# Kernel tuning notes

Measured on AMD Instinct MI355X. Metric: run time of the kernel, lower is better.

Reference implementation:

```python
import jax, jax.numpy as jnp
import numpy as np

B, N, E, H = 4, 1024, 1024, 16
D = E // H

def setup_inputs() -> dict:
    key = jax.random.key(0)
    ks = jax.random.split(key, 5)
    return {
        "x": jax.random.normal(ks[0], (B, N, E), dtype=jnp.float32),
        "Wqkv": jax.random.normal(ks[1], (E, 3 * E), dtype=jnp.float32) * 0.02,
        "bqkv": jax.random.normal(ks[2], (3 * E,), dtype=jnp.float32) * 0.02,
        "Wfc": jax.random.normal(ks[3], (E, E), dtype=jnp.float32) * 0.02,
        "bfc": jax.random.normal(ks[4], (E,), dtype=jnp.float32) * 0.02,
    }

def reference(x, Wqkv, bqkv, Wfc, bfc):
    b, n, e = x.shape
    h, d = H, E // H
    qkv = x @ Wqkv + bqkv                      # [b, n, 3e]
    q, k, v = jnp.split(qkv, 3, axis=-1)       # each [b, n, e]
    # view to [b, n, h, d] then RAW reshape to [b, h, n, d] (faithful to original,
    # which uses .reshape, not transpose — mixes seq/head axes)
    q = q.reshape(b, n, h, d).reshape(b, h, n, d)
    k = k.reshape(b, n, h, d).reshape(b, h, n, d)
    v = v.reshape(b, n, h, d).reshape(b, h, n, d)
    scores = jnp.einsum('bhqd,bhkd->bhqk', q, k) / jnp.sqrt(jnp.float32(d))
    causal = jnp.triu(jnp.ones((n, n), dtype=bool), k=1)  # True above diagonal
    scores = jnp.where(causal, -jnp.inf, scores)
    attn = jax.nn.softmax(scores, axis=-1)
    out = jnp.einsum('bhqk,bhkd->bhqd', attn, v)          # [b, h, n, d]
    # raw reshape back to [b, n, h, d] then flatten heads (faithful)
    out = out.reshape(b, n, h, d).reshape(b, n, e)
    return out @ Wfc + bfc
```

## Files before the change

kernel.cpp:

```cpp
#include <hip/hip_runtime.h>


typedef __bf16 bf16x8 __attribute__((ext_vector_type(8)));
typedef float f32x4 __attribute__((ext_vector_type(4)));

#define QSCALE 0.18033688011112042f
#define DEFER_THR 11.0f

__device__ __forceinline__ unsigned short f2bf(float f) {
    unsigned u = __float_as_uint(f);
    u += 0x7fffu + ((u >> 16) & 1u);
    return (unsigned short)(u >> 16);
}

__device__ __forceinline__ unsigned cvtpk_bf16(float lo, float hi) {
    unsigned r;
    asm("v_cvt_pk_bf16_f32 %0, %1, %2" : "=v"(r) : "v"(lo), "v"(hi));
    return r;
}

union FragU { uint4 u; bf16x8 v; };

__device__ __forceinline__ bf16x8 ld_frag(const unsigned short* p) {
    FragU x; x.u = *(const uint4*)p; return x.v;
}

__device__ __forceinline__ void gload_lds16(const void* g, void* l) {
    __builtin_amdgcn_global_load_lds(
        (const __attribute__((address_space(1))) void*)g,
        (__attribute__((address_space(3))) void*)l, 16, 0, 0);
}

__global__ __launch_bounds__(256) void prep(
    const float* __restrict__ x,    unsigned short* __restrict__ xb,
    const float* __restrict__ Wqkv, unsigned short* __restrict__ wqkvT,
    const float* __restrict__ Wfc,  unsigned short* __restrict__ wfcT)
{
    __shared__ float tile[32][33];
    int bid = blockIdx.x;
    int tx = threadIdx.x & 31, ty = threadIdx.x >> 5;
    if (bid < 3072) {
        int c0 = (bid % 96) * 32, r0 = (bid / 96) * 32;
        for (int i = ty; i < 32; i += 8)
            tile[i][tx] = Wqkv[(r0 + i) * 3072 + c0 + tx];
        __syncthreads();
        for (int i = ty; i < 32; i += 8)
            wqkvT[(long)(c0 + i) * 1024 + r0 + tx] = f2bf(tile[tx][i]);
    } else if (bid < 4096) {
        int b2 = bid - 3072;
        int c0 = (b2 % 32) * 32, r0 = (b2 / 32) * 32;
        for (int i = ty; i < 32; i += 8)
            tile[i][tx] = Wfc[(r0 + i) * 1024 + c0 + tx];
        __syncthreads();
        for (int i = ty; i < 32; i += 8)
            wfcT[(long)(c0 + i) * 1024 + r0 + tx] = f2bf(tile[tx][i]);
    } else {
        const int n4 = 1 << 20;
        for (int i = (bid - 4096) * 256 + threadIdx.x; i < n4; i += 1024 * 256) {
            float4 f = ((const float4*)x)[i];
            unsigned a = (unsigned)f2bf(f.x) | ((unsigned)f2bf(f.y) << 16);
            unsigned b = (unsigned)f2bf(f.z) | ((unsigned)f2bf(f.w) << 16);
            ((uint2*)xb)[i] = make_uint2(a, b);
        }
    }
}

__global__ void transpose_v(const unsigned short* __restrict__ v,
                            unsigned short* __restrict__ vt) {
    __shared__ unsigned short tile[32][33];
    int bh = blockIdx.z;
    int n0 = blockIdx.x * 32, d0 = blockIdx.y * 32;
    const unsigned short* src = v + (long)bh * 65536;
    unsigned short* dst = vt + (long)bh * 65536;
    for (int i = threadIdx.y; i < 32; i += 8)
        tile[i][threadIdx.x] = src[(n0 + i) * 64 + d0 + threadIdx.x];
    __syncthreads();
    for (int i = threadIdx.y; i < 32; i += 8)
        dst[(d0 + i) * 1024 + n0 + threadIdx.x] = tile[threadIdx.x][i];
}

template <int MODE>
__global__ __launch_bounds__(256) void gemm128(
    const unsigned short* __restrict__ A,
    const unsigned short* __restrict__ Bt,
    const float* __restrict__ bias,
    unsigned short* __restrict__ qb,
    unsigned short* __restrict__ kb,
    unsigned short* __restrict__ vb,
    float* __restrict__ outf)
{
    __shared__ unsigned short As[2][4096];
    __shared__ unsigned short Bs[2][4096];
    int t = threadIdx.x, lane = t & 63, w = t >> 6;
    int wm = w >> 1, wn = w & 1;
    int lrow = lane >> 4, lcol = lane & 15;

    const int NX  = (MODE == 0) ? 24 : 8;
    const int CPX = (MODE == 0) ? 96 : 32;
    int id = blockIdx.x;
    int idp = (id & 7) * CPX + (id >> 3);
    int tn0 = (idp % NX) * 128, tm0 = (idp / NX) * 128;

    int seg0 = w * 1024;
    int seg1 = (w + 4) * 1024;
    int off0 = seg0 + lane * 16, off1 = seg1 + lane * 16;
    int r0 = off0 >> 6, g0 = ((((off0 >> 4) & 3) ^ ((r0 >> 1) & 3)) << 4);
    int r1 = off1 >> 6, g1 = ((((off1 >> 4) & 3) ^ ((r1 >> 1) & 3)) << 4);

    const char* gA = (const char*)A;
    const char* gB = (const char*)Bt;

    int aoff[4], boff[4];
    #pragma unroll
    for (int mi = 0; mi < 4; ++mi) {
        int row = wm * 64 + mi * 16 + lcol;
        aoff[mi] = row * 32 + ((lrow ^ ((row >> 1) & 3)) << 3);
    }
    #pragma unroll
    for (int ni = 0; ni < 4; ++ni) {
        int row = wn * 64 + ni * 16 + lcol;
        boff[ni] = row * 32 + ((lrow ^ ((row >> 1) & 3)) << 3);
    }

    f32x4 acc[4][4] = {};

    auto STAGE = [&](int buf, int kt) {
        long kby = (long)kt * 2;
        gload_lds16(gA + (long)(tm0 + r0) * 2048 + kby + g0, (char*)&As[buf][0] + seg0);
        gload_lds16(gA + (long)(tm0 + r1) * 2048 + kby + g1, (char*)&As[buf][0] + seg1);
        gload_lds16(gB + (long)(tn0 + r0) * 2048 + kby + g0, (char*)&Bs[buf][0] + seg0);
        gload_lds16(gB + (long)(tn0 + r1) * 2048 + kby + g1, (char*)&Bs[buf][0] + seg1);
    };

    STAGE(0, 0);
    STAGE(1, 32);

    for (int tt = 0; tt < 32; ++tt) {
        if (tt < 31) asm volatile("s_waitcnt vmcnt(4)" ::: "memory");
        else         asm volatile("s_waitcnt vmcnt(0)" ::: "memory");
        __builtin_amdgcn_s_barrier();

        int cur = tt & 1;
        bf16x8 af[4], bfr[4];
        #pragma unroll
        for (int mi = 0; mi < 4; ++mi) af[mi] = ld_frag(&As[cur][aoff[mi]]);
        #pragma unroll
        for (int ni = 0; ni < 4; ++ni) bfr[ni] = ld_frag(&Bs[cur][boff[ni]]);
        #pragma unroll
        for (int mi = 0; mi < 4; ++mi)
            #pragma unroll
            for (int ni = 0; ni < 4; ++ni)
                acc[mi][ni] = __builtin_amdgcn_mfma_f32_16x16x32_bf16(af[mi], bfr[ni], acc[mi][ni], 0, 0, 0);

        __builtin_amdgcn_s_barrier();
        if (tt + 2 < 32) STAGE(cur, (tt + 2) * 32);
    }

    #pragma unroll
    for (int mi = 0; mi < 4; ++mi) {
        int gr0 = tm0 + wm * 64 + mi * 16 + lrow * 4;
        #pragma unroll
        for (int ni = 0; ni < 4; ++ni) {
            int gc = tn0 + wn * 64 + ni * 16 + lcol;
            float bv = bias[gc];
            if (MODE == 0) {
                int sec = gc >> 10, ei = gc & 1023;
                unsigned short* dst = sec == 0 ? qb : (sec == 1 ? kb : vb);
                if (sec == 0) {
                    #pragma unroll
                    for (int r = 0; r < 4; ++r)
                        dst[(long)(gr0 + r) * 1024 + ei] = f2bf((acc[mi][ni][r] + bv) * QSCALE);
                } else {
                    #pragma unroll
                    for (int r = 0; r < 4; ++r)
                        dst[(long)(gr0 + r) * 1024 + ei] = f2bf(acc[mi][ni][r] + bv);
                }
            } else {
                #pragma unroll
                for (int r = 0; r < 4; ++r)
                    outf[(long)(gr0 + r) * 1024 + gc] = acc[mi][ni][r] + bv;
            }
        }
    }
}

__global__ __launch_bounds__(256) void attn(
    const unsigned short* __restrict__ qbuf,
    const unsigned short* __restrict__ kbuf,
    const unsigned short* __restrict__ vtbuf,
    unsigned short* __restrict__ obuf)
{
    __shared__ unsigned short Ks[2][4096];
    __shared__ unsigned short Vs[2][4096];
    __shared__ unsigned short Ps[4][32][40];

    int id = blockIdx.x;
    int xcd = id & 7, s_ = id >> 3;
    int j  = 7 - (s_ >> 3);
    int bh = xcd + 8 * (s_ & 7);

    const char* Kb = (const char*)(kbuf + (long)bh * 65536);
    const char* Vb = (const char*)(vtbuf + (long)bh * 65536);
    const unsigned short* Q = qbuf + (long)bh * 65536;
    unsigned short* O = obuf + (long)bh * 65536;

    int t = threadIdx.x, lane = t & 63, w = t >> 6;
    int lrow = lane >> 4, lcol = lane & 15;
    const float NEG = -__builtin_inff();

    int qbase = j * 128 + w * 32;
    int T = 2 * j + 2;

    int row0 = w * 8 + (lane >> 3);
    int slot = (((lane & 7) ^ (lane >> 3)) << 4);

    auto STAGE = [&](int buf, int kt) {
        long k2 = (long)kt * 2;
        gload_lds16(Kb + (k2 + row0 * 2) * 64 + slot,        (char*)&Ks[buf][0] + w * 1024);
        gload_lds16(Kb + (k2 + (row0 + 32) * 2) * 64 + slot, (char*)&Ks[buf][0] + 4096 + w * 1024);
        gload_lds16(Vb + (long)row0 * 2048 + k2 + slot,        (char*)&Vs[buf][0] + w * 1024);
        gload_lds16(Vb + (long)(row0 + 32) * 2048 + k2 + slot, (char*)&Vs[buf][0] + 4096 + w * 1024);
    };

    bf16x8 qf[2][2];
    #pragma unroll
    for (int qg = 0; qg < 2; ++qg)
        #pragma unroll
        for (int kc = 0; kc < 2; ++kc)
            qf[qg][kc] = ld_frag(Q + (long)(qbase + qg * 16 + lcol) * 64 + kc * 32 + lrow * 8);

    f32x4 acc[2][4] = {};
    float m_i[2] = {NEG, NEG};
    float lsum[2][2] = {{0.f, 0.f}, {0.f, 0.f}};

    STAGE(0, 0);
    STAGE(1, 64);

    for (int tt = 0; tt < T; ++tt) {
        if (tt + 1 < T) asm volatile("s_waitcnt vmcnt(4)" ::: "memory");
        else            asm volatile("s_waitcnt vmcnt(0)" ::: "memory");
        __builtin_amdgcn_s_barrier();

        int cur = tt & 1;
        #pragma unroll
        for (int ks = 0; ks < 2; ++ks) {
            int kt_sub = tt * 64 + ks * 32;
            if (kt_sub <= qbase) {
                bf16x8 kf[2][2], vf[4];
                #pragma unroll
                for (int kg = 0; kg < 2; ++kg)
                    #pragma unroll
                    for (int kc = 0; kc < 2; ++kc) {
                        int row = ks * 32 + kg * 16 + lcol;
                        kf[kg][kc] = ld_frag(&Ks[cur][row * 64 + (((kc * 4 + lrow) ^ (row & 7)) << 3)]);
                    }
                #pragma unroll
                for (int dg = 0; dg < 4; ++dg) {
                    int row = dg * 16 + lcol;
                    vf[dg] = ld_frag(&Vs[cur][row * 64 + (((ks * 4 + lrow) ^ (row & 7)) << 3)]);
                }

                f32x4 s[2][2] = {};
                __builtin_amdgcn_s_setprio(1);
                #pragma unroll
                for (int kg = 0; kg < 2; ++kg)
                    #pragma unroll
                    for (int kc = 0; kc < 2; ++kc) {
                        s[0][kg] = __builtin_amdgcn_mfma_f32_16x16x32_bf16(kf[kg][kc], qf[0][kc], s[0][kg], 0, 0, 0);
                        s[1][kg] = __builtin_amdgcn_mfma_f32_16x16x32_bf16(kf[kg][kc], qf[1][kc], s[1][kg], 0, 0, 0);
                    }
                __builtin_amdgcn_s_setprio(0);

                bool diag = (kt_sub == qbase);
                if (diag) {
                    #pragma unroll
                    for (int qg = 0; qg < 2; ++qg)
                        #pragma unroll
                        for (int kg = 0; kg < 2; ++kg)
                            #pragma unroll
                            for (int r = 0; r < 4; ++r)
                                if (kg * 16 + lrow * 4 + r > qg * 16 + lcol)
                                    s[qg][kg][r] = NEG;
                }
                float lmax[2];
                #pragma unroll
                for (int qg = 0; qg < 2; ++qg) {
                    float a0 = fmaxf(s[qg][0][0], s[qg][0][1]), a1 = fmaxf(s[qg][0][2], s[qg][0][3]);
                    float a2 = fmaxf(s[qg][1][0], s[qg][1][1]), a3 = fmaxf(s[qg][1][2], s[qg][1][3]);
                    lmax[qg] = fmaxf(fmaxf(a0, a1), fmaxf(a2, a3));
                }
                bool ok = (lmax[0] <= m_i[0] + DEFER_THR) && (lmax[1] <= m_i[1] + DEFER_THR);
                if (!__all(ok)) {
                    #pragma unroll
                    for (int qg = 0; qg < 2; ++qg) {
                        float mx = fmaxf(lmax[qg], __shfl_xor(lmax[qg], 16));
                        mx = fmaxf(mx, __shfl_xor(mx, 32));
                        float mnew = fmaxf(m_i[qg], mx);
                        float alpha = exp2f(m_i[qg] - mnew);
                        m_i[qg] = mnew;
                        lsum[qg][0] *= alpha;
                        lsum[qg][1] *= alpha;
                        #pragma unroll
                        for (int dg = 0; dg < 4; ++dg)
                            #pragma unroll
                            for (int r = 0; r < 4; ++r)
                                acc[qg][dg][r] *= alpha;
                    }
                }
                #pragma unroll
                for (int qg = 0; qg < 2; ++qg) {
                    float p[8];
                    #pragma unroll
                    for (int kg = 0; kg < 2; ++kg)
                        #pragma unroll
                        for (int r = 0; r < 4; ++r)
                            p[kg * 4 + r] = exp2f(s[qg][kg][r] - m_i[qg]);
                    lsum[qg][0] += (p[0] + p[1]) + (p[2] + p[3]);
                    lsum[qg][1] += (p[4] + p[5]) + (p[6] + p[7]);
                    unsigned u0 = cvtpk_bf16(p[0], p[1]);
                    unsigned u1 = cvtpk_bf16(p[2], p[3]);
                    unsigned u2 = cvtpk_bf16(p[4], p[5]);
                    unsigned u3 = cvtpk_bf16(p[6], p[7]);
                    *(uint2*)&Ps[w][qg * 16 + lcol][lrow * 4]      = make_uint2(u0, u1);
                    *(uint2*)&Ps[w][qg * 16 + lcol][16 + lrow * 4] = make_uint2(u2, u3);
                }

                bf16x8 pb[2];
                pb[0] = ld_frag(&Ps[w][lcol][lrow * 8]);
                pb[1] = ld_frag(&Ps[w][16 + lcol][lrow * 8]);

                __builtin_amdgcn_s_setprio(1);
                #pragma unroll
                for (int dg = 0; dg < 4; ++dg) {
                    acc[0][dg] = __builtin_amdgcn_mfma_f32_16x16x32_bf16(vf[dg], pb[0], acc[0][dg], 0, 0, 0);
                    acc[1][dg] = __builtin_amdgcn_mfma_f32_16x16x32_bf16(vf[dg], pb[1], acc[1][dg], 0, 0, 0);
                }
                __builtin_amdgcn_s_setprio(0);
            }
        }

        __builtin_amdgcn_s_barrier();
        if (tt + 2 < T) STAGE(cur, (tt + 2) * 64);
    }

    #pragma unroll
    for (int qg = 0; qg < 2; ++qg) {
        float lr = lsum[qg][0] + lsum[qg][1];
        lr += __shfl_xor(lr, 16);
        lr += __shfl_xor(lr, 32);
        float inv = 1.f / lr;
        int q = qbase + qg * 16 + lcol;
        #pragma unroll
        for (int dg = 0; dg < 4; ++dg) {
            ushort4 pk;
            pk.x = f2bf(acc[qg][dg][0] * inv);
            pk.y = f2bf(acc[qg][dg][1] * inv);
            pk.z = f2bf(acc[qg][dg][2] * inv);
            pk.w = f2bf(acc[qg][dg][3] * inv);
            *(ushort4*)&O[(long)q * 64 + dg * 16 + lrow * 4] = pk;
        }
    }
}

extern "C" void kernel_launch(void* const* d_in, const int* in_sizes, int n_in,
                              void* d_out, int out_size, void* d_ws, size_t ws_size,
                              hipStream_t stream) {
    const float* x    = (const float*)d_in[0];
    const float* Wqkv = (const float*)d_in[1];
    const float* bqkv = (const float*)d_in[2];
    const float* Wfc  = (const float*)d_in[3];
    const float* bfc  = (const float*)d_in[4];
    float* out = (float*)d_out;

    unsigned short* ws    = (unsigned short*)d_ws;
    unsigned short* xb    = ws;
    unsigned short* wqkvT = xb + (4u << 20);
    unsigned short* wfcT  = wqkvT + (3u << 20);
    unsigned short* qb    = wfcT + (1u << 20);
    unsigned short* kb    = qb + (4u << 20);
    unsigned short* vb    = kb + (4u << 20);
    unsigned short* vbT   = xb;
    unsigned short* ob    = vb;

    prep<<<dim3(5120), dim3(256), 0, stream>>>(x, xb, Wqkv, wqkvT, Wfc, wfcT);
    gemm128<0><<<dim3(768), dim3(256), 0, stream>>>(xb, wqkvT, bqkv, qb, kb, vb, nullptr);
    transpose_v<<<dim3(32, 2, 64), dim3(32, 8), 0, stream>>>(vb, vbT);
    attn<<<dim3(512), dim3(256), 0, stream>>>(qb, kb, vbT, ob);
    gemm128<1><<<dim3(256), dim3(256), 0, stream>>>(ob, wfcT, bfc, nullptr, nullptr, nullptr, out);
}
```

Before: 112.6 us.

## Load GEMM A operand directly from global into registers, bypassing LDS

The GEMM kernel no longer stages the A tile through shared memory. Each wave now loads its A fragments straight from global memory into registers, prefetching one k-step ahead. B stays double-buffered in LDS, and the vmcnt wait counts are adjusted for the extra in-flight loads. This halves LDS footprint and LDS read traffic, but A is fetched twice, once per wn wave, and with less coalesced 64-byte row segments, so L2 and global traffic for A rises.

```diff
diff --git a/kernel.cpp b/kernel.cpp
--- a/kernel.cpp
+++ b/kernel.cpp
@@ -89,7 +89,6 @@
     unsigned short* __restrict__ vb,
     float* __restrict__ outf)
 {
-    __shared__ unsigned short As[2][4096];
     __shared__ unsigned short Bs[2][4096];
     int t = threadIdx.x, lane = t & 63, w = t >> 6;
     int wm = w >> 1, wn = w & 1;
@@ -101,49 +100,53 @@
     int idp = (id & 7) * CPX + (id >> 3);
     int tn0 = (idp % NX) * 128, tm0 = (idp / NX) * 128;
 
-    int seg0 = w * 1024;
-    int seg1 = (w + 4) * 1024;
-    int off0 = seg0 + lane * 16, off1 = seg1 + lane * 16;
+    int off0 = w * 1024 + lane * 16;
+    int off1 = 4096 + w * 1024 + lane * 16;
     int r0 = off0 >> 6, g0 = ((((off0 >> 4) & 3) ^ ((r0 >> 1) & 3)) << 4);
     int r1 = off1 >> 6, g1 = ((((off1 >> 4) & 3) ^ ((r1 >> 1) & 3)) << 4);
-
-    const char* gA = (const char*)A;
-    const char* gB = (const char*)Bt;
-
-    int aoff[4], boff[4];
-    #pragma unroll
-    for (int mi = 0; mi < 4; ++mi) {
-        int row = wm * 64 + mi * 16 + lcol;
-        aoff[mi] = row * 32 + ((lrow ^ ((row >> 1) & 3)) << 3);
-    }
+    const char* pB0 = (const char*)Bt + (long)(tn0 + r0) * 2048 + g0;
+    const char* pB1 = (const char*)Bt + (long)(tn0 + r1) * 2048 + g1;
+
+    int boff[4];
     #pragma unroll
     for (int ni = 0; ni < 4; ++ni) {
         int row = wn * 64 + ni * 16 + lcol;
         boff[ni] = row * 32 + ((lrow ^ ((row >> 1) & 3)) << 3);
     }
 
+    const unsigned short* pAg[4];
+    #pragma unroll
+    for (int mi = 0; mi < 4; ++mi)
+        pAg[mi] = A + (long)(tm0 + wm * 64 + mi * 16 + lcol) * 1024 + lrow * 8;
+
     f32x4 acc[4][4] = {};
 
     auto STAGE = [&](int buf, int kt) {
         long kby = (long)kt * 2;
-        gload_lds16(gA + (long)(tm0 + r0) * 2048 + kby + g0, (char*)&As[buf][0] + seg0);
-        gload_lds16(gA + (long)(tm0 + r1) * 2048 + kby + g1, (char*)&As[buf][0] + seg1);
-        gload_lds16(gB + (long)(tn0 + r0) * 2048 + kby + g0, (char*)&Bs[buf][0] + seg0);
-        gload_lds16(gB + (long)(tn0 + r1) * 2048 + kby + g1, (char*)&Bs[buf][0] + seg1);
+        gload_lds16(pB0 + kby, (char*)&Bs[buf][0] + w * 1024);
+        gload_lds16(pB1 + kby, (char*)&Bs[buf][0] + 4096 + w * 1024);
     };
 
     STAGE(0, 0);
     STAGE(1, 32);
+    bf16x8 af[4];
+    #pragma unroll
+    for (int mi = 0; mi < 4; ++mi) af[mi] = ld_frag(pAg[mi]);
 
     for (int tt = 0; tt < 32; ++tt) {
-        if (tt < 31) asm volatile("s_waitcnt vmcnt(4)" ::: "memory");
-        else         asm volatile("s_waitcnt vmcnt(0)" ::: "memory");
+        if (tt < 31) asm volatile("s_waitcnt vmcnt(6)" ::: "memory");
+        else         asm volatile("s_waitcnt vmcnt(4)" ::: "memory");
         __builtin_amdgcn_s_barrier();
 
+        bf16x8 afn[4];
+        if (tt < 31) {
+            #pragma unroll
+            for (int mi = 0; mi < 4; ++mi)
+                afn[mi] = ld_frag(pAg[mi] + (tt + 1) * 32);
+        }
+
         int cur = tt & 1;
-        bf16x8 af[4], bfr[4];
-        #pragma unroll
-        for (int mi = 0; mi < 4; ++mi) af[mi] = ld_frag(&As[cur][aoff[mi]]);
+        bf16x8 bfr[4];
         #pragma unroll
         for (int ni = 0; ni < 4; ++ni) bfr[ni] = ld_frag(&Bs[cur][boff[ni]]);
         #pragma unroll
@@ -154,6 +157,9 @@
 
         __builtin_amdgcn_s_barrier();
         if (tt + 2 < 32) STAGE(cur, (tt + 2) * 32);
+
+        #pragma unroll
+        for (int mi = 0; mi < 4; ++mi) af[mi] = afn[mi];
     }
 
     #pragma unroll
```

New measurement: 156.8 us. +39.2%, slower.

## Halve attention query tile to 64 rows per block, doubling grid size

Applied to the files above, without the earlier changes.

The attention kernel now gives each wave 16 query rows instead of 32, so a block covers 64 queries and the grid grows from 512 to 1024 blocks. Causal masking becomes a general partial-tile test instead of an exact diagonal match. This is meant to improve occupancy and load balance across the causal triangle, at the cost of re-streaming K/V tiles twice as often per query. The GEMM also precomputes its per-thread global load base pointers once, removing repeated address arithmetic inside the staging loop.

```diff
diff --git a/kernel.cpp b/kernel.cpp
--- a/kernel.cpp
+++ b/kernel.cpp
@@ -101,14 +101,15 @@
     int idp = (id & 7) * CPX + (id >> 3);
     int tn0 = (idp % NX) * 128, tm0 = (idp / NX) * 128;
 
-    int seg0 = w * 1024;
-    int seg1 = (w + 4) * 1024;
-    int off0 = seg0 + lane * 16, off1 = seg1 + lane * 16;
-    int r0 = off0 >> 6, g0 = ((((off0 >> 4) & 3) ^ ((r0 >> 1) & 3)) << 4);
-    int r1 = off1 >> 6, g1 = ((((off1 >> 4) & 3) ^ ((r1 >> 1) & 3)) << 4);
-
-    const char* gA = (const char*)A;
-    const char* gB = (const char*)Bt;
+    int off0 = w * 1024 + lane * 16, off1 = 4096 + w * 1024 + lane * 16;
+    int r0 = (off0 & 4095) >> 6, g0 = ((((off0 >> 4) & 3) ^ ((r0 >> 1) & 3)) << 4);
+    int r1 = (off1 & 4095) >> 6, g1 = ((((off1 >> 4) & 3) ^ ((r1 >> 1) & 3)) << 4);
+    r1 += 64;
+
+    const char* pA0 = (const char*)A  + (long)(tm0 + r0) * 2048 + g0;
+    const char* pA1 = (const char*)A  + (long)(tm0 + r1) * 2048 + g1;
+    const char* pB0 = (const char*)Bt + (long)(tn0 + r0) * 2048 + g0;
+    const char* pB1 = (const char*)Bt + (long)(tn0 + r1) * 2048 + g1;
 
     int aoff[4], boff[4];
     #pragma unroll
@@ -126,10 +127,10 @@
 
     auto STAGE = [&](int buf, int kt) {
         long kby = (long)kt * 2;
-        gload_lds16(gA + (long)(tm0 + r0) * 2048 + kby + g0, (char*)&As[buf][0] + seg0);
-        gload_lds16(gA + (long)(tm0 + r1) * 2048 + kby + g1, (char*)&As[buf][0] + seg1);
-        gload_lds16(gB + (long)(tn0 + r0) * 2048 + kby + g0, (char*)&Bs[buf][0] + seg0);
-        gload_lds16(gB + (long)(tn0 + r1) * 2048 + kby + g1, (char*)&Bs[buf][0] + seg1);
+        gload_lds16(pA0 + kby, (char*)&As[buf][0] + w * 1024);
+        gload_lds16(pA1 + kby, (char*)&As[buf][0] + 4096 + w * 1024);
+        gload_lds16(pB0 + kby, (char*)&Bs[buf][0] + w * 1024);
+        gload_lds16(pB1 + kby, (char*)&Bs[buf][0] + 4096 + w * 1024);
     };
 
     STAGE(0, 0);
@@ -192,11 +193,11 @@
 {
     __shared__ unsigned short Ks[2][4096];
     __shared__ unsigned short Vs[2][4096];
-    __shared__ unsigned short Ps[4][32][40];
+    __shared__ unsigned short Ps[4][16][40];
 
     int id = blockIdx.x;
     int xcd = id & 7, s_ = id >> 3;
-    int j  = 7 - (s_ >> 3);
+    int j  = 15 - (s_ >> 3);
     int bh = xcd + 8 * (s_ & 7);
 
     const char* Kb = (const char*)(kbuf + (long)bh * 65536);
@@ -208,8 +209,8 @@
     int lrow = lane >> 4, lcol = lane & 15;
     const float NEG = -__builtin_inff();
 
-    int qbase = j * 128 + w * 32;
-    int T = 2 * j + 2;
+    int qbase = j * 64 + w * 16;
+    int T = j + 1;
 
     int row0 = w * 8 + (lane >> 3);
     int slot = (((lane & 7) ^ (lane >> 3)) << 4);
@@ -222,16 +223,14 @@
         gload_lds16(Vb + (long)(row0 + 32) * 2048 + k2 + slot, (char*)&Vs[buf][0] + 4096 + w * 1024);
     };
 
-    bf16x8 qf[2][2];
+    bf16x8 qf[2];
     #pragma unroll
-    for (int qg = 0; qg < 2; ++qg)
-        #pragma unroll
-        for (int kc = 0; kc < 2; ++kc)
-            qf[qg][kc] = ld_frag(Q + (long)(qbase + qg * 16 + lcol) * 64 + kc * 32 + lrow * 8);
-
-    f32x4 acc[2][4] = {};
-    float m_i[2] = {NEG, NEG};
-    float lsum[2][2] = {{0.f, 0.f}, {0.f, 0.f}};
+    for (int kc = 0; kc < 2; ++kc)
+        qf[kc] = ld_frag(Q + (long)(qbase + lcol) * 64 + kc * 32 + lrow * 8);
+
+    f32x4 acc[4] = {};
+    float m_i = NEG;
+    float l0 = 0.f, l1 = 0.f;
 
     STAGE(0, 0);
     STAGE(1, 64);
@@ -245,7 +244,7 @@
         #pragma unroll
         for (int ks = 0; ks < 2; ++ks) {
             int kt_sub = tt * 64 + ks * 32;
-            if (kt_sub <= qbase) {
+            if (kt_sub < qbase + 16) {
                 bf16x8 kf[2][2], vf[4];
                 #pragma unroll
                 for (int kg = 0; kg < 2; ++kg)
@@ -260,81 +259,61 @@
                     vf[dg] = ld_frag(&Vs[cur][row * 64 + (((ks * 4 + lrow) ^ (row & 7)) << 3)]);
                 }
 
-                f32x4 s[2][2] = {};
+                f32x4 s[2] = {};
                 __builtin_amdgcn_s_setprio(1);
                 #pragma unroll
                 for (int kg = 0; kg < 2; ++kg)
                     #pragma unroll
-                    for (int kc = 0; kc < 2; ++kc) {
-                        s[0][kg] = __builtin_amdgcn_mfma_f32_16x16x32_bf16(kf[kg][kc], qf[0][kc], s[0][kg], 0, 0, 0);
-                        s[1][kg] = __builtin_amdgcn_mfma_f32_16x16x32_bf16(kf[kg][kc], qf[1][kc], s[1][kg], 0, 0, 0);
-                    }
+                    for (int kc = 0; kc < 2; ++kc)
+                        s[kg] = __builtin_amdgcn_mfma_f32_16x16x32_bf16(kf[kg][kc], qf[kc], s[kg], 0, 0, 0);
                 __builtin_amdgcn_s_setprio(0);
 
-                bool diag = (kt_sub == qbase);
-                if (diag) {
-                    #pragma unroll
-                    for (int qg = 0; qg < 2; ++qg)
-                        #pragma unroll
-                        for (int kg = 0; kg < 2; ++kg)
-                            #pragma unroll
-                            for (int r = 0; r < 4; ++r)
-                                if (kg * 16 + lrow * 4 + r > qg * 16 + lcol)
-                                    s[qg][kg][r] = NEG;
-                }
-                float lmax[2];
-                #pragma unroll
-                for (int qg = 0; qg < 2; ++qg) {
-                    float a0 = fmaxf(s[qg][0][0], s[qg][0][1]), a1 = fmaxf(s[qg][0][2], s[qg][0][3]);
-                    float a2 = fmaxf(s[qg][1][0], s[qg][1][1]), a3 = fmaxf(s[qg][1][2], s[qg][1][3]);
-                    lmax[qg] = fmaxf(fmaxf(a0, a1), fmaxf(a2, a3));
-                }
-                bool ok = (lmax[0] <= m_i[0] + DEFER_THR) && (lmax[1] <= m_i[1] + DEFER_THR);
-                if (!__all(ok)) {
-                    #pragma unroll
-                    for (int qg = 0; qg < 2; ++qg) {
-                        float mx = fmaxf(lmax[qg], __shfl_xor(lmax[qg], 16));
-                        mx = fmaxf(mx, __shfl_xor(mx, 32));
-                        float mnew = fmaxf(m_i[qg], mx);
-                        float alpha = exp2f(m_i[qg] - mnew);
-                        m_i[qg] = mnew;
-                        lsum[qg][0] *= alpha;
-                        lsum[qg][1] *= alpha;
-                        #pragma unroll
-                        for (int dg = 0; dg < 4; ++dg)
-                            #pragma unroll
-                            for (int r = 0; r < 4; ++r)
-                                acc[qg][dg][r] *= alpha;
-                    }
-                }
-                #pragma unroll
-                for (int qg = 0; qg < 2; ++qg) {
-                    float p[8];
+                if (kt_sub + 31 > qbase) {
                     #pragma unroll
                     for (int kg = 0; kg < 2; ++kg)
                         #pragma unroll
                         for (int r = 0; r < 4; ++r)
-                            p[kg * 4 + r] = exp2f(s[qg][kg][r] - m_i[qg]);
-                    lsum[qg][0] += (p[0] + p[1]) + (p[2] + p[3]);
-                    lsum[qg][1] += (p[4] + p[5]) + (p[6] + p[7]);
-                    unsigned u0 = cvtpk_bf16(p[0], p[1]);
-                    unsigned u1 = cvtpk_bf16(p[2], p[3]);
-                    unsigned u2 = cvtpk_bf16(p[4], p[5]);
-                    unsigned u3 = cvtpk_bf16(p[6], p[7]);
-                    *(uint2*)&Ps[w][qg * 16 + lcol][lrow * 4]      = make_uint2(u0, u1);
-                    *(uint2*)&Ps[w][qg * 16 + lcol][16 + lrow * 4] = make_uint2(u2, u3);
+                            if (kt_sub + kg * 16 + lrow * 4 + r > qbase + lcol)
+                                s[kg][r] = NEG;
                 }
-
-                bf16x8 pb[2];
-                pb[0] = ld_frag(&Ps[w][lcol][lrow * 8]);
-                pb[1] = ld_frag(&Ps[w][16 + lcol][lrow * 8]);
+                float a0 = fmaxf(s[0][0], s[0][1]), a1 = fmaxf(s[0][2], s[0][3]);
+                float a2 = fmaxf(s[1][0], s[1][1]), a3 = fmaxf(s[1][2], s[1][3]);
+                float lmax = fmaxf(fmaxf(a0, a1), fmaxf(a2, a3));
+                bool ok = (lmax <= m_i + DEFER_THR);
+                if (!__all(ok)) {
+                    float mx = fmaxf(lmax, __shfl_xor(lmax, 16));
+                    mx = fmaxf(mx, __shfl_xor(mx, 32));
+                    float mnew = fmaxf(m_i, mx);
+                    float alpha = exp2f(m_i - mnew);
+                    m_i = mnew;
+                    l0 *= alpha; l1 *= alpha;
+                    #pragma unroll
+                    for (int dg = 0; dg < 4; ++dg)
+                        #pragma unroll
+                        for (int r = 0; r < 4; ++r)
+                            acc[dg][r] *= alpha;
+                }
+                float p[8];
+                #pragma unroll
+                for (int kg = 0; kg < 2; ++kg)
+                    #pragma unroll
+                    for (int r = 0; r < 4; ++r)
+                        p[kg * 4 + r] = exp2f(s[kg][r] - m_i);
+                l0 += (p[0] + p[1]) + (p[2] + p[3]);
+                l1 += (p[4] + p[5]) + (p[6] + p[7]);
+                unsigned u0 = cvtpk_bf16(p[0], p[1]);
+                unsigned u1 = cvtpk_bf16(p[2], p[3]);
+                unsigned u2 = cvtpk_bf16(p[4], p[5]);
+                unsigned u3 = cvtpk_bf16(p[6], p[7]);
+                *(uint2*)&Ps[w][lcol][lrow * 4]      = make_uint2(u0, u1);
+                *(uint2*)&Ps[w][lcol][16 + lrow * 4] = make_uint2(u2, u3);
+
+                bf16x8 pb = ld_frag(&Ps[w][lcol][lrow * 8]);
 
                 __builtin_amdgcn_s_setprio(1);
                 #pragma unroll
-                for (int dg = 0; dg < 4; ++dg) {
-                    acc[0][dg] = __builtin_amdgcn_mfma_f32_16x16x32_bf16(vf[dg], pb[0], acc[0][dg], 0, 0, 0);
-                    acc[1][dg] = __builtin_amdgcn_mfma_f32_16x16x32_bf16(vf[dg], pb[1], acc[1][dg], 0, 0, 0);
-                }
+                for (int dg = 0; dg < 4; ++dg)
+                    acc[dg] = __builtin_amdgcn_mfma_f32_16x16x32_bf16(vf[dg], pb, acc[dg], 0, 0, 0);
                 __builtin_amdgcn_s_setprio(0);
             }
         }
@@ -343,20 +322,19 @@
         if (tt + 2 < T) STAGE(cur, (tt + 2) * 64);
     }
 
-    #pragma unroll
-    for (int qg = 0; qg < 2; ++qg) {
-        float lr = lsum[qg][0] + lsum[qg][1];
+    {
+        float lr = l0 + l1;
         lr += __shfl_xor(lr, 16);
         lr += __shfl_xor(lr, 32);
         float inv = 1.f / lr;
-        int q = qbase + qg * 16 + lcol;
+        int q = qbase + lcol;
         #pragma unroll
         for (int dg = 0; dg < 4; ++dg) {
             ushort4 pk;
-            pk.x = f2bf(acc[qg][dg][0] * inv);
-            pk.y = f2bf(acc[qg][dg][1] * inv);
-            pk.z = f2bf(acc[qg][dg][2] * inv);
-            pk.w = f2bf(acc[qg][dg][3] * inv);
+            pk.x = f2bf(acc[dg][0] * inv);
+            pk.y = f2bf(acc[dg][1] * inv);
+            pk.z = f2bf(acc[dg][2] * inv);
+            pk.w = f2bf(acc[dg][3] * inv);
             *(ushort4*)&O[(long)q * 64 + dg * 16 + lrow * 4] = pk;
         }
     }
@@ -385,6 +363,6 @@
     prep<<<dim3(5120), dim3(256), 0, stream>>>(x, xb, Wqkv, wqkvT, Wfc, wfcT);
     gemm128<0><<<dim3(768), dim3(256), 0, stream>>>(xb, wqkvT, bqkv, qb, kb, vb, nullptr);
     transpose_v<<<dim3(32, 2, 64), dim3(32, 8), 0, stream>>>(vb, vbT);
-    attn<<<dim3(512), dim3(256), 0, stream>>>(qb, kb, vbT, ob);
+    attn<<<dim3(1024), dim3(256), 0, stream>>>(qb, kb, vbT, ob);
     gemm128<1><<<dim3(256), dim3(256), 0, stream>>>(ob, wfcT, bfc, nullptr, nullptr, nullptr, out);
 }
```

New measurement: 104.7 us. -7.1%, faster.
